# Kernel optimization log

Measured on AMD Instinct MI355X. Metric: run time of the kernel, lower is better.

The kernel has to match this reference:

```python
import jax, jax.numpy as jnp
import numpy as np
from jax import lax
from jax.scipy.special import logsumexp

NUM_TAGS = 5
B, L = 16384, 512


def setup_inputs() -> dict:
    key = jax.random.key(0)
    k1, k2, k3, k4, k5 = jax.random.split(key, 5)
    emissions = jax.random.normal(k1, (B, L, NUM_TAGS), dtype=jnp.float32)
    tags = jax.random.randint(k2, (B, L), 0, NUM_TAGS)
    mask = jnp.ones((B, L), dtype=bool)
    # learned CRF parameters, init U(-0.1, 0.1) as in reset_parameters
    transitions = jax.random.uniform(k3, (NUM_TAGS, NUM_TAGS), minval=-0.1, maxval=0.1, dtype=jnp.float32)
    start_transitions = jax.random.uniform(k4, (NUM_TAGS,), minval=-0.1, maxval=0.1, dtype=jnp.float32)
    end_transitions = jax.random.uniform(k5, (NUM_TAGS,), minval=-0.1, maxval=0.1, dtype=jnp.float32)
    return {
        "emissions": emissions,
        "transitions": transitions,
        "start_transitions": start_transitions,
        "end_transitions": end_transitions,
        "tags": tags,
        "mask": mask,
    }


def reference(emissions, transitions, start_transitions, end_transitions, tags, mask):
    """CRF mean negative log-likelihood: log_partition - gold_score (both batch means)."""
    Bs, Ls, C = emissions.shape
    maskf = mask.astype(emissions.dtype)

    # ---- log partition (forward algorithm); note: original torch code's
    # mask application here is a no-op (where(mask, s, s)), reproduced faithfully.
    init_score = start_transitions[None, :] + emissions[:, 0]  # (B, C)

    def step(score, em_i):
        # score: (B, C) over previous tag; em_i: (B, C)
        nxt = logsumexp(score[:, :, None] + transitions[None, :, :] + em_i[:, None, :], axis=1)
        return nxt, None

    ems = jnp.swapaxes(emissions[:, 1:], 0, 1)  # (L-1, B, C)
    final_score, _ = lax.scan(step, init_score, ems)
    log_den = logsumexp(final_score + end_transitions[None, :], axis=1).mean()

    # ---- gold path score (fully vectorized over time)
    s0 = start_transitions[tags[:, 0]] + jnp.take_along_axis(emissions[:, 0], tags[:, :1], axis=1)[:, 0]
    trans_scores = transitions[tags[:, :-1], tags[:, 1:]]  # (B, L-1)
    em_at_tags = jnp.take_along_axis(emissions, tags[:, :, None], axis=2)[:, :, 0]  # (B, L)
    path_score = s0 + ((trans_scores + em_at_tags[:, 1:]) * maskf[:, 1:]).sum(axis=1)
    last_idx = mask.sum(axis=1).astype(jnp.int32) - 1  # (B,)
    last_tags = jnp.take_along_axis(tags, last_idx[:, None], axis=1)[:, 0]
    log_num = (path_score + end_transitions[last_tags]).mean()

    return log_den - log_num
```

## Files before the change

kernel.cpp:

```cpp
#include <hip/hip_runtime.h>

#define NTAGS 5
#define BATCH 16384
#define SEQL 512
#define CL 8
#define SEQF (SEQL * NTAGS)
#define PADC 41
#define SEQPF (64 * PADC)
#define PTAG 9
#define SEQPT (64 * PTAG)
#define NREC 16
#define RECF 28

__device__ __forceinline__ float sel5v(float a0, float a1, float a2, float a3, float a4, int t) {
    float r = a0;
    r = (t == 1) ? a1 : r;
    r = (t == 2) ? a2 : r;
    r = (t == 3) ? a3 : r;
    r = (t == 4) ? a4 : r;
    return r;
}
__device__ __forceinline__ float f4c(float4 v, int c) {
    switch (c & 3) { case 0: return v.x; case 1: return v.y; case 2: return v.z; default: return v.w; }
}

__global__ __launch_bounds__(256, 2) void crf_phase1(
    const float* __restrict__ emis, const float* __restrict__ trans,
    const float* __restrict__ startT, const int* __restrict__ tags,
    float* __restrict__ ws) {
    __shared__ float lemis[4 * SEQPF];
    __shared__ int ltags[4 * SEQPT];
    __shared__ float ldsT[25];

    const int tid = threadIdx.x;
    const int lane = tid & 63;
    const int wid = tid >> 6;

    const float4* ge = (const float4*)(emis + (size_t)blockIdx.x * 4 * SEQF);
#pragma unroll
    for (int w = 0; w < 10; ++w) {
        const int f = w * 256 + tid;
        const float4 v = ge[f];
        const int F = 4 * f;
        const int s = F / SEQF;
        const int r = F - s * SEQF;
        const int piece = r / 40;
        const int off = r - piece * 40;
        float* dst = &lemis[s * SEQPF + piece * PADC + off];
        dst[0] = v.x; dst[1] = v.y; dst[2] = v.z; dst[3] = v.w;
    }
    const int4* gt4 = (const int4*)(tags + (size_t)blockIdx.x * 4 * SEQL);
#pragma unroll
    for (int w = 0; w < 2; ++w) {
        const int g = w * 256 + tid;
        const int4 v = gt4[g];
        const int T = 4 * g;
        const int s = T >> 9;
        const int q = T & 511;
        const int piece = q >> 3;
        const int j = q & 7;
        int* dst = &ltags[s * SEQPT + piece * PTAG + j];
        dst[0] = v.x; dst[1] = v.y; dst[2] = v.z; dst[3] = v.w;
    }
    if (tid < 25) ldsT[tid] = trans[tid];
    __syncthreads();

    float eT[25];
#pragma unroll
    for (int i = 0; i < 25; ++i) eT[i] = __expf(trans[i]);
    float stR[5];
#pragma unroll
    for (int j = 0; j < 5; ++j) stR[j] = startT[j];

    const float* E = &lemis[wid * SEQPF + lane * PADC];
    const int* G = &ltags[wid * SEQPT + lane * PTAG];

    float path = 0.f;
    int prev = (lane == 0) ? 0 : G[7 - PTAG];
#pragma unroll
    for (int t = 0; t < CL; ++t) {
        const int tag = G[t];
        const float et = E[t * 5 + tag];
        if (lane == 0 && t == 0) {
            path += sel5v(stR[0], stR[1], stR[2], stR[3], stR[4], tag) + et;
        } else {
            path += ldsT[prev * 5 + tag] + et;
        }
        prev = tag;
    }

    float M[25];
    float logS = 0.f;
    const int bump = (lane == 0) ? 1 : 0;
    {
        const float* e = &E[bump * 5];
        const float x0 = __expf(e[0]), x1 = __expf(e[1]), x2 = __expf(e[2]),
                    x3 = __expf(e[3]), x4 = __expf(e[4]);
#pragma unroll
        for (int i = 0; i < 5; ++i) {
            M[i * 5 + 0] = eT[i * 5 + 0] * x0;
            M[i * 5 + 1] = eT[i * 5 + 1] * x1;
            M[i * 5 + 2] = eT[i * 5 + 2] * x2;
            M[i * 5 + 3] = eT[i * 5 + 3] * x3;
            M[i * 5 + 4] = eT[i * 5 + 4] * x4;
        }
    }
#pragma unroll
    for (int u = 1; u < CL; ++u) {
        const int s = u + bump;
        if (s < CL) {
            const float* e = &E[s * 5];
            const float ex0 = __expf(e[0]), ex1 = __expf(e[1]), ex2 = __expf(e[2]),
                        ex3 = __expf(e[3]), ex4 = __expf(e[4]);
#pragma unroll
            for (int i = 0; i < 5; ++i) {
                const float m0 = M[i * 5 + 0], m1 = M[i * 5 + 1], m2 = M[i * 5 + 2],
                            m3 = M[i * 5 + 3], m4 = M[i * 5 + 4];
#pragma unroll
                for (int j = 0; j < 5; ++j) {
                    float a = m0 * eT[j];
                    a = fmaf(m1, eT[5 + j], a);
                    a = fmaf(m2, eT[10 + j], a);
                    a = fmaf(m3, eT[15 + j], a);
                    a = fmaf(m4, eT[20 + j], a);
                    const float exj = (j == 0) ? ex0 : (j == 1) ? ex1 : (j == 2) ? ex2
                                     : (j == 3) ? ex3 : ex4;
                    M[i * 5 + j] = a * exj;
                }
            }
        }
    }
    {
        float mx = M[0];
#pragma unroll
        for (int i = 1; i < 25; ++i) mx = fmaxf(mx, M[i]);
        logS += __logf(mx);
        const float rc = __builtin_amdgcn_rcpf(mx);
#pragma unroll
        for (int i = 0; i < 25; ++i) M[i] *= rc;
    }

#pragma unroll
    for (int lvl = 0; lvl < 2; ++lvl) {
        const int mk = 1 << lvl;
        float O[25];
#pragma unroll
        for (int i = 0; i < 25; ++i) O[i] = __shfl_xor(M[i], mk, 64);
        const float oS = __shfl_xor(logS, mk, 64);
        const bool hi = (lane & mk) != 0;
        float L[25], R[25];
#pragma unroll
        for (int i = 0; i < 25; ++i) {
            L[i] = hi ? O[i] : M[i];
            R[i] = hi ? M[i] : O[i];
        }
#pragma unroll
        for (int i = 0; i < 5; ++i)
#pragma unroll
            for (int j = 0; j < 5; ++j) {
                float a = L[i * 5 + 0] * R[0 * 5 + j];
                a = fmaf(L[i * 5 + 1], R[1 * 5 + j], a);
                a = fmaf(L[i * 5 + 2], R[2 * 5 + j], a);
                a = fmaf(L[i * 5 + 3], R[3 * 5 + j], a);
                a = fmaf(L[i * 5 + 4], R[4 * 5 + j], a);
                M[i * 5 + j] = a;
            }
        logS += oS;
    }
    {
        float mx = M[0];
#pragma unroll
        for (int i = 1; i < 25; ++i) mx = fmaxf(mx, M[i]);
        logS += __logf(mx);
        const float rc = __builtin_amdgcn_rcpf(mx);
#pragma unroll
        for (int i = 0; i < 25; ++i) M[i] *= rc;
    }
    path += __shfl_xor(path, 1, 64);
    path += __shfl_xor(path, 2, 64);

    float* rb = &lemis[wid * SEQPF];
    if ((lane & 3) == 0) {
        float* r = &rb[(lane >> 2) * RECF];
#pragma unroll
        for (int i = 0; i < 25; ++i) r[i] = M[i];
        r[25] = logS;
        r[26] = path;
        r[27] = 0.f;
    }
    __syncthreads();
    float4* wdst = (float4*)(ws + (size_t)blockIdx.x * (4 * NREC * RECF));
    {
        const int F = 4 * tid;
        const int s = F / 448;
        const int r = F - s * 448;
        wdst[tid] = *(const float4*)&lemis[s * SEQPF + r];
        if (tid < 192) {
            const int k = 256 + tid;
            const int F2 = 4 * k;
            const int s2 = F2 / 448;
            const int r2 = F2 - s2 * 448;
            wdst[k] = *(const float4*)&lemis[s2 * SEQPF + r2];
        }
    }
}

__device__ __forceinline__ void p2_combine(const float4 r[7], float v[5], float& logZ,
                                           float& path) {
#define MM(i, j) f4c(r[((i) * 5 + (j)) >> 2], ((i) * 5 + (j)) & 3)
    float nv[5];
#pragma unroll
    for (int j = 0; j < 5; ++j) {
        float a = v[0] * MM(0, j);
        a = fmaf(v[1], MM(1, j), a);
        a = fmaf(v[2], MM(2, j), a);
        a = fmaf(v[3], MM(3, j), a);
        a = fmaf(v[4], MM(4, j), a);
        nv[j] = a;
    }
#undef MM
    logZ += r[6].y;
    path += r[6].z;
    const float m = fmaxf(fmaxf(fmaxf(nv[0], nv[1]), fmaxf(nv[2], nv[3])), nv[4]);
    logZ += __logf(m);
    const float rc = __builtin_amdgcn_rcpf(m);
#pragma unroll
    for (int j = 0; j < 5; ++j) v[j] = nv[j] * rc;
}

__global__ __launch_bounds__(64) void crf_phase2(
    const float* __restrict__ emis, const float* __restrict__ startT,
    const float* __restrict__ endT, const int* __restrict__ tags,
    const float* __restrict__ ws, float* __restrict__ out) {
    const int seq = blockIdx.x * 64 + threadIdx.x;
    const float* eb = emis + (size_t)seq * (SEQL * NTAGS);
    const float4* wsb = (const float4*)(ws + (size_t)seq * NREC * RECF);

    float4 r[4][7];
#pragma unroll
    for (int s = 0; s < 4; ++s)
#pragma unroll
        for (int k = 0; k < 7; ++k) r[s][k] = wsb[s * 7 + k];

    const float4 e03 = *(const float4*)eb;
    const float e4v = eb[4];
    const float s0 = startT[0] + e03.x, s1 = startT[1] + e03.y, s2 = startT[2] + e03.z,
                s3 = startT[3] + e03.w, s4 = startT[4] + e4v;
    const float m0 = fmaxf(fmaxf(fmaxf(s0, s1), fmaxf(s2, s3)), s4);
    float v[5] = {__expf(s0 - m0), __expf(s1 - m0), __expf(s2 - m0), __expf(s3 - m0),
                  __expf(s4 - m0)};
    float logZ = m0, path = 0.f;

#pragma unroll
    for (int c = 0; c < NREC; ++c) {
        p2_combine(r[c & 3], v, logZ, path);
        if (c + 4 < NREC) {
#pragma unroll
            for (int k = 0; k < 7; ++k) r[c & 3][k] = wsb[(c + 4) * 7 + k];
        }
    }

    const float en0 = endT[0], en1 = endT[1], en2 = endT[2], en3 = endT[3], en4 = endT[4];
    float sden = v[0] * __expf(en0);
    sden = fmaf(v[1], __expf(en1), sden);
    sden = fmaf(v[2], __expf(en2), sden);
    sden = fmaf(v[3], __expf(en3), sden);
    sden = fmaf(v[4], __expf(en4), sden);
    const float den = logZ + __logf(sden);

    const int lastTag = tags[seq * SEQL + (SEQL - 1)];
    const float num = path + sel5v(en0, en1, en2, en3, en4, lastTag);

    float val = (den - num) * (1.0f / (float)BATCH);
#pragma unroll
    for (int off = 32; off > 0; off >>= 1) val += __shfl_xor(val, off, 64);
    if (threadIdx.x == 0) atomicAdd(out, val);
}

extern "C" void kernel_launch(void* const* d_in, const int* in_sizes, int n_in,
                              void* d_out, int out_size, void* d_ws, size_t ws_size,
                              hipStream_t stream) {
    const float* emis = (const float*)d_in[0];
    const float* trans = (const float*)d_in[1];
    const float* startT = (const float*)d_in[2];
    const float* endT = (const float*)d_in[3];
    const int* tags = (const int*)d_in[4];
    float* out = (float*)d_out;
    float* ws = (float*)d_ws;

    hipMemsetAsync(out, 0, sizeof(float), stream);
    crf_phase1<<<dim3(BATCH / 4), dim3(256), 0, stream>>>(emis, trans, startT, tags, ws);
    crf_phase2<<<dim3(BATCH / 64), dim3(64), 0, stream>>>(emis, startT, endT, tags, ws,
                                                          out);
}
```

Baseline: 296.4 us.

## Shrink phase-1 blocks, load tags directly, and write records straight to workspace

Phase-1 blocks shrink from 4 to 2 sequences (128 threads), which halves shared memory per block and raises the allowed blocks per CU. Tags are now read straight from global memory into registers as two int4 loads per lane, with the previous tag obtained by a lane shuffle, so the tags LDS staging disappears. Each lane copies its 40 emissions from LDS into registers once, and the gold-path score is folded into the matrix-product loop. Lane 0 now uses an identity matrix in place of the special bump case, and the final records go to global memory as float4 stores without the extra LDS pass and second barrier, at the cost of more register pressure.

Result: faster. 290.3 us (-2.1%).

```diff
diff --git a/kernel.cpp b/kernel.cpp
--- a/kernel.cpp
+++ b/kernel.cpp
@@ -7,8 +7,6 @@
 #define SEQF (SEQL * NTAGS)
 #define PADC 41
 #define SEQPF (64 * PADC)
-#define PTAG 9
-#define SEQPT (64 * PTAG)
 #define NREC 16
 #define RECF 28
 
@@ -24,22 +22,21 @@
     switch (c & 3) { case 0: return v.x; case 1: return v.y; case 2: return v.z; default: return v.w; }
 }
 
-__global__ __launch_bounds__(256, 2) void crf_phase1(
+__global__ __launch_bounds__(128, 3) void crf_phase1(
     const float* __restrict__ emis, const float* __restrict__ trans,
     const float* __restrict__ startT, const int* __restrict__ tags,
     float* __restrict__ ws) {
-    __shared__ float lemis[4 * SEQPF];
-    __shared__ int ltags[4 * SEQPT];
+    __shared__ float lemis[2 * SEQPF];
     __shared__ float ldsT[25];
 
     const int tid = threadIdx.x;
     const int lane = tid & 63;
     const int wid = tid >> 6;
 
-    const float4* ge = (const float4*)(emis + (size_t)blockIdx.x * 4 * SEQF);
+    const float4* ge = (const float4*)(emis + (size_t)blockIdx.x * 2 * SEQF);
 #pragma unroll
     for (int w = 0; w < 10; ++w) {
-        const int f = w * 256 + tid;
+        const int f = w * 128 + tid;
         const float4 v = ge[f];
         const int F = 4 * f;
         const int s = F / SEQF;
@@ -49,86 +46,81 @@
         float* dst = &lemis[s * SEQPF + piece * PADC + off];
         dst[0] = v.x; dst[1] = v.y; dst[2] = v.z; dst[3] = v.w;
     }
-    const int4* gt4 = (const int4*)(tags + (size_t)blockIdx.x * 4 * SEQL);
-#pragma unroll
-    for (int w = 0; w < 2; ++w) {
-        const int g = w * 256 + tid;
-        const int4 v = gt4[g];
-        const int T = 4 * g;
-        const int s = T >> 9;
-        const int q = T & 511;
-        const int piece = q >> 3;
-        const int j = q & 7;
-        int* dst = &ltags[s * SEQPT + piece * PTAG + j];
-        dst[0] = v.x; dst[1] = v.y; dst[2] = v.z; dst[3] = v.w;
-    }
     if (tid < 25) ldsT[tid] = trans[tid];
+
+    float eT[25];
+#pragma unroll
+    for (int i = 0; i < 25; ++i) eT[i] = __expf(trans[i]);
+
+    const int seq = blockIdx.x * 2 + wid;
+    const int4* tsrc = (const int4*)(tags + (size_t)seq * SEQL + lane * CL);
+    const int4 g0 = tsrc[0], g1 = tsrc[1];
+    const int tg0 = g0.x, tg1 = g0.y, tg2 = g0.z, tg3 = g0.w;
+    const int tg4 = g1.x, tg5 = g1.y, tg6 = g1.z, tg7 = g1.w;
+    int prev = __shfl_up(g1.w, 1, 64);
+
+    float stR[5];
+#pragma unroll
+    for (int j = 0; j < 5; ++j) stR[j] = startT[j];
+
     __syncthreads();
 
-    float eT[25];
-#pragma unroll
-    for (int i = 0; i < 25; ++i) eT[i] = __expf(trans[i]);
-    float stR[5];
-#pragma unroll
-    for (int j = 0; j < 5; ++j) stR[j] = startT[j];
-
-    const float* E = &lemis[wid * SEQPF + lane * PADC];
-    const int* G = &ltags[wid * SEQPT + lane * PTAG];
-
-    float path = 0.f;
-    int prev = (lane == 0) ? 0 : G[7 - PTAG];
-#pragma unroll
-    for (int t = 0; t < CL; ++t) {
-        const int tag = G[t];
-        const float et = E[t * 5 + tag];
-        if (lane == 0 && t == 0) {
-            path += sel5v(stR[0], stR[1], stR[2], stR[3], stR[4], tag) + et;
-        } else {
-            path += ldsT[prev * 5 + tag] + et;
-        }
+    const float* Eb = &lemis[wid * SEQPF + lane * PADC];
+    float R[40];
+#pragma unroll
+    for (int k = 0; k < 40; ++k) R[k] = Eb[k];
+
+    const bool l0 = (lane == 0);
+    float path;
+    {
+        const int tag = tg0;
+        const float esel = sel5v(R[0], R[1], R[2], R[3], R[4], tag);
+        const float stsel = sel5v(stR[0], stR[1], stR[2], stR[3], stR[4], tag);
+        const float trv = ldsT[prev * 5 + tag];
+        path = (l0 ? stsel : trv) + esel;
         prev = tag;
     }
-
     float M[25];
+    {
+        const float x0 = __expf(R[0]), x1 = __expf(R[1]), x2 = __expf(R[2]),
+                    x3 = __expf(R[3]), x4 = __expf(R[4]);
+#pragma unroll
+        for (int i = 0; i < 5; ++i) {
+            M[i * 5 + 0] = l0 ? ((i == 0) ? 1.f : 0.f) : eT[i * 5 + 0] * x0;
+            M[i * 5 + 1] = l0 ? ((i == 1) ? 1.f : 0.f) : eT[i * 5 + 1] * x1;
+            M[i * 5 + 2] = l0 ? ((i == 2) ? 1.f : 0.f) : eT[i * 5 + 2] * x2;
+            M[i * 5 + 3] = l0 ? ((i == 3) ? 1.f : 0.f) : eT[i * 5 + 3] * x3;
+            M[i * 5 + 4] = l0 ? ((i == 4) ? 1.f : 0.f) : eT[i * 5 + 4] * x4;
+        }
+    }
+
     float logS = 0.f;
-    const int bump = (lane == 0) ? 1 : 0;
-    {
-        const float* e = &E[bump * 5];
-        const float x0 = __expf(e[0]), x1 = __expf(e[1]), x2 = __expf(e[2]),
-                    x3 = __expf(e[3]), x4 = __expf(e[4]);
+#pragma unroll
+    for (int s = 1; s < CL; ++s) {
+        const float e0 = R[s * 5 + 0], e1 = R[s * 5 + 1], e2 = R[s * 5 + 2],
+                    e3 = R[s * 5 + 3], e4 = R[s * 5 + 4];
+        const int tag = (s == 1) ? tg1 : (s == 2) ? tg2 : (s == 3) ? tg3 : (s == 4) ? tg4
+                       : (s == 5) ? tg5 : (s == 6) ? tg6 : tg7;
+        const float ex0 = __expf(e0), ex1 = __expf(e1), ex2 = __expf(e2),
+                    ex3 = __expf(e3), ex4 = __expf(e4);
 #pragma unroll
         for (int i = 0; i < 5; ++i) {
-            M[i * 5 + 0] = eT[i * 5 + 0] * x0;
-            M[i * 5 + 1] = eT[i * 5 + 1] * x1;
-            M[i * 5 + 2] = eT[i * 5 + 2] * x2;
-            M[i * 5 + 3] = eT[i * 5 + 3] * x3;
-            M[i * 5 + 4] = eT[i * 5 + 4] * x4;
-        }
-    }
-#pragma unroll
-    for (int u = 1; u < CL; ++u) {
-        const int s = u + bump;
-        if (s < CL) {
-            const float* e = &E[s * 5];
-            const float ex0 = __expf(e[0]), ex1 = __expf(e[1]), ex2 = __expf(e[2]),
-                        ex3 = __expf(e[3]), ex4 = __expf(e[4]);
-#pragma unroll
-            for (int i = 0; i < 5; ++i) {
-                const float m0 = M[i * 5 + 0], m1 = M[i * 5 + 1], m2 = M[i * 5 + 2],
-                            m3 = M[i * 5 + 3], m4 = M[i * 5 + 4];
-#pragma unroll
-                for (int j = 0; j < 5; ++j) {
-                    float a = m0 * eT[j];
-                    a = fmaf(m1, eT[5 + j], a);
-                    a = fmaf(m2, eT[10 + j], a);
-                    a = fmaf(m3, eT[15 + j], a);
-                    a = fmaf(m4, eT[20 + j], a);
-                    const float exj = (j == 0) ? ex0 : (j == 1) ? ex1 : (j == 2) ? ex2
-                                     : (j == 3) ? ex3 : ex4;
-                    M[i * 5 + j] = a * exj;
-                }
+            const float m0 = M[i * 5 + 0], m1 = M[i * 5 + 1], m2 = M[i * 5 + 2],
+                        m3 = M[i * 5 + 3], m4 = M[i * 5 + 4];
+#pragma unroll
+            for (int j = 0; j < 5; ++j) {
+                float a = m0 * eT[j];
+                a = fmaf(m1, eT[5 + j], a);
+                a = fmaf(m2, eT[10 + j], a);
+                a = fmaf(m3, eT[15 + j], a);
+                a = fmaf(m4, eT[20 + j], a);
+                const float exj = (j == 0) ? ex0 : (j == 1) ? ex1 : (j == 2) ? ex2
+                                 : (j == 3) ? ex3 : ex4;
+                M[i * 5 + j] = a * exj;
             }
         }
+        path += ldsT[prev * 5 + tag] + sel5v(e0, e1, e2, e3, e4, tag);
+        prev = tag;
     }
     {
         float mx = M[0];
@@ -148,21 +140,21 @@
         for (int i = 0; i < 25; ++i) O[i] = __shfl_xor(M[i], mk, 64);
         const float oS = __shfl_xor(logS, mk, 64);
         const bool hi = (lane & mk) != 0;
-        float L[25], R[25];
+        float L[25], Rm[25];
 #pragma unroll
         for (int i = 0; i < 25; ++i) {
             L[i] = hi ? O[i] : M[i];
-            R[i] = hi ? M[i] : O[i];
+            Rm[i] = hi ? M[i] : O[i];
         }
 #pragma unroll
         for (int i = 0; i < 5; ++i)
 #pragma unroll
             for (int j = 0; j < 5; ++j) {
-                float a = L[i * 5 + 0] * R[0 * 5 + j];
-                a = fmaf(L[i * 5 + 1], R[1 * 5 + j], a);
-                a = fmaf(L[i * 5 + 2], R[2 * 5 + j], a);
-                a = fmaf(L[i * 5 + 3], R[3 * 5 + j], a);
-                a = fmaf(L[i * 5 + 4], R[4 * 5 + j], a);
+                float a = L[i * 5 + 0] * Rm[0 * 5 + j];
+                a = fmaf(L[i * 5 + 1], Rm[1 * 5 + j], a);
+                a = fmaf(L[i * 5 + 2], Rm[2 * 5 + j], a);
+                a = fmaf(L[i * 5 + 3], Rm[3 * 5 + j], a);
+                a = fmaf(L[i * 5 + 4], Rm[4 * 5 + j], a);
                 M[i * 5 + j] = a;
             }
         logS += oS;
@@ -179,29 +171,15 @@
     path += __shfl_xor(path, 1, 64);
     path += __shfl_xor(path, 2, 64);
 
-    float* rb = &lemis[wid * SEQPF];
     if ((lane & 3) == 0) {
-        float* r = &rb[(lane >> 2) * RECF];
-#pragma unroll
-        for (int i = 0; i < 25; ++i) r[i] = M[i];
-        r[25] = logS;
-        r[26] = path;
-        r[27] = 0.f;
-    }
-    __syncthreads();
-    float4* wdst = (float4*)(ws + (size_t)blockIdx.x * (4 * NREC * RECF));
-    {
-        const int F = 4 * tid;
-        const int s = F / 448;
-        const int r = F - s * 448;
-        wdst[tid] = *(const float4*)&lemis[s * SEQPF + r];
-        if (tid < 192) {
-            const int k = 256 + tid;
-            const int F2 = 4 * k;
-            const int s2 = F2 / 448;
-            const int r2 = F2 - s2 * 448;
-            wdst[k] = *(const float4*)&lemis[s2 * SEQPF + r2];
-        }
+        float4* rp = (float4*)(ws + ((size_t)seq * NREC + (lane >> 2)) * RECF);
+        rp[0] = make_float4(M[0], M[1], M[2], M[3]);
+        rp[1] = make_float4(M[4], M[5], M[6], M[7]);
+        rp[2] = make_float4(M[8], M[9], M[10], M[11]);
+        rp[3] = make_float4(M[12], M[13], M[14], M[15]);
+        rp[4] = make_float4(M[16], M[17], M[18], M[19]);
+        rp[5] = make_float4(M[20], M[21], M[22], M[23]);
+        rp[6] = make_float4(M[24], logS, path, 0.f);
     }
 }
 
@@ -289,7 +267,7 @@
     float* ws = (float*)d_ws;
 
     hipMemsetAsync(out, 0, sizeof(float), stream);
-    crf_phase1<<<dim3(BATCH / 4), dim3(256), 0, stream>>>(emis, trans, startT, tags, ws);
+    crf_phase1<<<dim3(BATCH / 2), dim3(128), 0, stream>>>(emis, trans, startT, tags, ws);
     crf_phase2<<<dim3(BATCH / 64), dim3(64), 0, stream>>>(emis, startT, endT, tags, ws,
                                                           out);
 }
```
